# Performance work log

Measured on AMD Instinct MI355X. Metric: run time of the kernel, lower is better.

Reference implementation:

```python
import jax, jax.numpy as jnp
import numpy as np

TEMPERATURE = 0.5
EPS = 1e-8  # torch.nn.CosineSimilarity default eps


def setup_inputs() -> dict:
    key = jax.random.key(0)
    k1, k2 = jax.random.split(key)
    B, D = 4096, 256
    z1 = jax.random.normal(k1, (B, D), dtype=jnp.float32)
    # z2 = perturbed view of z1 so positive cosine sims are positive
    # (original torch code takes log of the RAW cosine sim, which is NaN
    #  for negative positives; realistic SimCLR positives are correlated views)
    z2 = z1 + 0.1 * jax.random.normal(k2, (B, D), dtype=jnp.float32)
    return {"z1": z1, "z2": z2}


def reference(z1, z2):
    B = z1.shape[0]
    z = jnp.concatenate([z1, z2], axis=0)                      # [2B, D]
    norm = jnp.maximum(jnp.linalg.norm(z, axis=-1, keepdims=True), EPS)
    zn = z / norm
    sim = zn @ zn.T                                            # [2B, 2B] cosine sims
    # positives: sim[i, i+B] and sim[i+B, i] (RAW cosine, per original code)
    pos = jnp.concatenate([jnp.diagonal(sim, offset=B),
                           jnp.diagonal(sim, offset=-B)])      # [2B]
    # mask self-similarity diagonal to -inf before exp-sum
    diag = jnp.eye(2 * B, dtype=bool)
    sim_masked = jnp.where(diag, -jnp.inf, sim)
    denom = jnp.sum(jnp.exp(sim_masked / TEMPERATURE), axis=-1)  # [2B]
    loss = -jnp.mean(jnp.log(pos / denom))
    return loss
```

## Files before the change

### kernel.cpp

```cpp
#include <hip/hip_runtime.h>
#include <hip/hip_bf16.h>


#define NROWS 8192
#define BHALF 4096
#define DDIM  256

typedef __attribute__((ext_vector_type(4))) int   i32x4;
typedef __attribute__((ext_vector_type(8))) int   i32x8;
typedef __attribute__((ext_vector_type(4))) float f32x4;

#define SCALE1 0x7F7F7F7F
#define TWO_LOG2E 2.8853900817779268f

__device__ __forceinline__ void load_lds16(const unsigned char* g, unsigned char* l) {
    __builtin_amdgcn_global_load_lds(
        (const __attribute__((address_space(1))) void*)g,
        (__attribute__((address_space(3))) void*)l, 16, 0, 0);
}

__global__ __launch_bounds__(256) void prep_kernel(const float* __restrict__ z1,
                                                   const float* __restrict__ z2,
                                                   unsigned char* __restrict__ zn8,
                                                   float* __restrict__ posPart,
                                                   float* __restrict__ denom,
                                                   float* __restrict__ out) {
    __shared__ float sp[4];
    int wave = threadIdx.x >> 6;
    int lane = threadIdx.x & 63;
    int i    = blockIdx.x * 4 + wave;
    float4 a = reinterpret_cast<const float4*>(z1 + (size_t)i * DDIM)[lane];
    float4 b = reinterpret_cast<const float4*>(z2 + (size_t)i * DDIM)[lane];
    float ss1 = a.x * a.x + a.y * a.y + a.z * a.z + a.w * a.w;
    float ss2 = b.x * b.x + b.y * b.y + b.z * b.z + b.w * b.w;
    float dd  = a.x * b.x + a.y * b.y + a.z * b.z + a.w * b.w;
    #pragma unroll
    for (int off = 32; off; off >>= 1) {
        ss1 += __shfl_xor(ss1, off);
        ss2 += __shfl_xor(ss2, off);
        dd  += __shfl_xor(dd, off);
    }
    float n1 = fmaxf(sqrtf(ss1), 1e-8f);
    float n2 = fmaxf(sqrtf(ss2), 1e-8f);
    float i1 = 1.0f / n1, i2 = 1.0f / n2;
    int pa = __builtin_amdgcn_cvt_pk_fp8_f32(a.x * i1, a.y * i1, 0, 0);
    pa     = __builtin_amdgcn_cvt_pk_fp8_f32(a.z * i1, a.w * i1, pa, 1);
    int pb = __builtin_amdgcn_cvt_pk_fp8_f32(b.x * i2, b.y * i2, 0, 0);
    pb     = __builtin_amdgcn_cvt_pk_fp8_f32(b.z * i2, b.w * i2, pb, 1);
    reinterpret_cast<int*>(zn8 + (size_t)i * DDIM)[lane] = pa;
    reinterpret_cast<int*>(zn8 + (size_t)(i + BHALF) * DDIM)[lane] = pb;
    if (lane == 0) sp[wave] = __logf(dd * i1 * i2);
    if (threadIdx.x < 8) denom[blockIdx.x * 8 + threadIdx.x] = 0.0f;
    if (blockIdx.x == 0 && threadIdx.x == 64) out[0] = 0.0f;
    __syncthreads();
    if (threadIdx.x == 0)
        posPart[blockIdx.x] = sp[0] + sp[1] + sp[2] + sp[3];
}

__global__ __launch_bounds__(256, 3) void denom_kernel(const unsigned char* __restrict__ zn8,
                                                       float* __restrict__ denom) {
    __shared__ __align__(16) unsigned char sMem[48 * 1024];
    unsigned char* sA  = sMem;
    unsigned char* sB0 = sMem + 32768;
    unsigned char* sB1 = sMem;

    int x = blockIdx.x, y = blockIdx.y;
    int bi, bj;
    if (x > y) { bi = y;      bj = x - 1;  }
    else       { bi = 63 - y; bj = 63 - x; }
    int iBase = bi * 128;
    int jBase = bj * 128;
    bool isDiag = (bi == bj);

    int t    = threadIdx.x;
    int lane = t & 63;
    int wave = t >> 6;
    int col  = lane & 15;
    int quad = lane >> 4;
    int wm = wave >> 1, wn = wave & 1;

    int rowL  = t >> 4;
    int chunk = (t & 15) ^ rowL;

    {
        const unsigned char* gA = zn8 + (size_t)(iBase + rowL) * DDIM + chunk * 16;
        #pragma unroll
        for (int q = 0; q < 8; q++)
            load_lds16(gA + q * 4096, sA + t * 16 + q * 4096);
        const unsigned char* gB = zn8 + (size_t)(jBase + rowL) * DDIM + chunk * 16;
        #pragma unroll
        for (int q = 0; q < 4; q++)
            load_lds16(gB + q * 4096, sB0 + t * 16 + q * 4096);
    }
    __syncthreads();

    i32x8 af[4][2];
    {
        const unsigned char* aRow = sA + (size_t)(wm * 64 + col) * DDIM;
        #pragma unroll
        for (int mt = 0; mt < 4; mt++)
            #pragma unroll
            for (int ks = 0; ks < 2; ks++) {
                int g0 = ks * 8 + quad * 2;
                i32x4 lo = *(const i32x4*)(aRow + mt * 16 * DDIM + ((g0    ) ^ col) * 16);
                i32x4 hi = *(const i32x4*)(aRow + mt * 16 * DDIM + ((g0 + 1) ^ col) * 16);
                af[mt][ks] = __builtin_shufflevector(lo, hi, 0, 1, 2, 3, 4, 5, 6, 7);
            }
    }
    __syncthreads();

    {
        const unsigned char* gB = zn8 + (size_t)(jBase + 64 + rowL) * DDIM + chunk * 16;
        #pragma unroll
        for (int q = 0; q < 4; q++)
            load_lds16(gB + q * 4096, sB1 + t * 16 + q * 4096);
    }

    float rs[4][4];
    #pragma unroll
    for (int mt = 0; mt < 4; mt++)
        #pragma unroll
        for (int r = 0; r < 4; r++) rs[mt][r] = 0.f;

    #pragma unroll
    for (int h = 0; h < 2; h++) {
        if (h) __syncthreads();
        const unsigned char* bRow =
            (h ? sB1 : sB0) + (size_t)(wn * 32 + col) * DDIM;

        i32x8 bfr[2][2];
        #pragma unroll
        for (int nt = 0; nt < 2; nt++)
            #pragma unroll
            for (int ks = 0; ks < 2; ks++) {
                int g0 = ks * 8 + quad * 2;
                i32x4 lo = *(const i32x4*)(bRow + nt * 16 * DDIM + ((g0    ) ^ col) * 16);
                i32x4 hi = *(const i32x4*)(bRow + nt * 16 * DDIM + ((g0 + 1) ^ col) * 16);
                bfr[nt][ks] = __builtin_shufflevector(lo, hi, 0, 1, 2, 3, 4, 5, 6, 7);
            }

        float cs[2] = {0.f, 0.f};
        #pragma unroll
        for (int mt = 0; mt < 4; mt++) {
            int gi = iBase + wm * 64 + mt * 16;
            #pragma unroll
            for (int nt = 0; nt < 2; nt++) {
                f32x4 acc = {0.f, 0.f, 0.f, 0.f};
                acc = __builtin_amdgcn_mfma_scale_f32_16x16x128_f8f6f4(
                          af[mt][0], bfr[nt][0], acc, 0, 0, 0, SCALE1, 0, SCALE1);
                acc = __builtin_amdgcn_mfma_scale_f32_16x16x128_f8f6f4(
                          af[mt][1], bfr[nt][1], acc, 0, 0, 0, SCALE1, 0, SCALE1);
                bool dtile = (gi == jBase + h * 64 + wn * 32 + nt * 16);
                float csl = 0.f;
                #pragma unroll
                for (int r = 0; r < 4; r++) {
                    float e = exp2f(acc[r] * TWO_LOG2E);
                    if (dtile && (quad * 4 + r) == col) e = 0.f;
                    rs[mt][r] += e;
                    csl += e;
                }
                cs[nt] += csl;
            }
        }

        if (!isDiag) {
            #pragma unroll
            for (int nt = 0; nt < 2; nt++) {
                float v = cs[nt];
                v += __shfl_xor(v, 16);
                v += __shfl_xor(v, 32);
                if (quad == 0)
                    atomicAdd(&denom[jBase + h * 64 + wn * 32 + nt * 16 + col], v);
            }
        }
    }

    #pragma unroll
    for (int mt = 0; mt < 4; mt++)
        #pragma unroll
        for (int r = 0; r < 4; r++) {
            float v = rs[mt][r];
            v += __shfl_xor(v, 1);
            v += __shfl_xor(v, 2);
            v += __shfl_xor(v, 4);
            v += __shfl_xor(v, 8);
            rs[mt][r] = v;
        }
    __syncthreads();
    float* red = (float*)(sMem + 16384);
    if (col == 0) {
        #pragma unroll
        for (int mt = 0; mt < 4; mt++)
            #pragma unroll
            for (int r = 0; r < 4; r++)
                red[wn * 128 + wm * 64 + mt * 16 + quad * 4 + r] = rs[mt][r];
    }
    __syncthreads();
    if (t < 128)
        atomicAdd(&denom[iBase + t], red[t] + red[128 + t]);
}

__global__ __launch_bounds__(256) void loss_kernel(const float* __restrict__ posPart,
                                                   const float* __restrict__ denom,
                                                   float* __restrict__ out) {
    __shared__ float sdata[4];
    int t = threadIdx.x;
    float s = __logf(denom[blockIdx.x * 256 + t]);
    if (t < 32) s -= 2.0f * posPart[blockIdx.x * 32 + t];
    #pragma unroll
    for (int off = 32; off; off >>= 1) s += __shfl_xor(s, off);
    if ((t & 63) == 0) sdata[t >> 6] = s;
    __syncthreads();
    if (t == 0)
        atomicAdd(out, (sdata[0] + sdata[1] + sdata[2] + sdata[3]) * (1.0f / NROWS));
}

extern "C" void kernel_launch(void* const* d_in, const int* in_sizes, int n_in,
                              void* d_out, int out_size, void* d_ws, size_t ws_size,
                              hipStream_t stream) {
    const float* z1 = (const float*)d_in[0];
    const float* z2 = (const float*)d_in[1];

    unsigned char* zn8 = (unsigned char*)d_ws;
    float* denom   = (float*)((char*)d_ws + (size_t)NROWS * DDIM);
    float* posPart = denom + NROWS;

    prep_kernel<<<BHALF / 4, 256, 0, stream>>>(z1, z2, zn8, posPart, denom, (float*)d_out);
    denom_kernel<<<dim3(65, 32), 256, 0, stream>>>(zn8, denom);
    loss_kernel<<<NROWS / 256, 256, 0, stream>>>(posPart, denom, (float*)d_out);
}
```

Measured before the change: 86.71 us.

## Replace global atomic denominator accumulation with per-tile partial sums array

```diff
diff --git a/kernel.cpp b/kernel.cpp
--- a/kernel.cpp
+++ b/kernel.cpp
@@ -23,7 +23,6 @@
                                                    const float* __restrict__ z2,
                                                    unsigned char* __restrict__ zn8,
                                                    float* __restrict__ posPart,
-                                                   float* __restrict__ denom,
                                                    float* __restrict__ out) {
     __shared__ float sp[4];
     int wave = threadIdx.x >> 6;
@@ -50,7 +49,6 @@
     reinterpret_cast<int*>(zn8 + (size_t)i * DDIM)[lane] = pa;
     reinterpret_cast<int*>(zn8 + (size_t)(i + BHALF) * DDIM)[lane] = pb;
     if (lane == 0) sp[wave] = __logf(dd * i1 * i2);
-    if (threadIdx.x < 8) denom[blockIdx.x * 8 + threadIdx.x] = 0.0f;
     if (blockIdx.x == 0 && threadIdx.x == 64) out[0] = 0.0f;
     __syncthreads();
     if (threadIdx.x == 0)
@@ -58,11 +56,13 @@
 }
 
 __global__ __launch_bounds__(256, 3) void denom_kernel(const unsigned char* __restrict__ zn8,
-                                                       float* __restrict__ denom) {
+                                                       float* __restrict__ P) {
     __shared__ __align__(16) unsigned char sMem[48 * 1024];
     unsigned char* sA  = sMem;
     unsigned char* sB0 = sMem + 32768;
     unsigned char* sB1 = sMem;
+    float* red    = (float*)(sMem + 16384);
+    float* colRed = red + 256;
 
     int x = blockIdx.x, y = blockIdx.y;
     int bi, bj;
@@ -170,7 +170,7 @@
                 v += __shfl_xor(v, 16);
                 v += __shfl_xor(v, 32);
                 if (quad == 0)
-                    atomicAdd(&denom[jBase + h * 64 + wn * 32 + nt * 16 + col], v);
+                    colRed[wm * 128 + h * 64 + wn * 32 + nt * 16 + col] = v;
             }
         }
     }
@@ -187,7 +187,6 @@
             rs[mt][r] = v;
         }
     __syncthreads();
-    float* red = (float*)(sMem + 16384);
     if (col == 0) {
         #pragma unroll
         for (int mt = 0; mt < 4; mt++)
@@ -196,16 +195,33 @@
                 red[wn * 128 + wm * 64 + mt * 16 + quad * 4 + r] = rs[mt][r];
     }
     __syncthreads();
-    if (t < 128)
-        atomicAdd(&denom[iBase + t], red[t] + red[128 + t]);
+    if (t < 128) {
+        float* Prow = P + (((size_t)bi * 64 + bj) << 7);
+        Prow[t] = red[t] + red[128 + t];
+        if (!isDiag) {
+            float* Pcol = P + (((size_t)bj * 64 + bi) << 7);
+            Pcol[t] = colRed[t] + colRed[128 + t];
+        }
+    }
 }
 
 __global__ __launch_bounds__(256) void loss_kernel(const float* __restrict__ posPart,
-                                                   const float* __restrict__ denom,
+                                                   const float* __restrict__ P,
                                                    float* __restrict__ out) {
     __shared__ float sdata[4];
     int t = threadIdx.x;
-    float s = __logf(denom[blockIdx.x * 256 + t]);
+    int i = blockIdx.x * 256 + t;
+    int bi = i >> 7, r = i & 127;
+    const float* p = P + ((size_t)bi << 13) + r;
+    float d0 = 0.f, d1 = 0.f, d2 = 0.f, d3 = 0.f;
+    #pragma unroll
+    for (int k = 0; k < 64; k += 4) {
+        d0 += p[(k + 0) << 7];
+        d1 += p[(k + 1) << 7];
+        d2 += p[(k + 2) << 7];
+        d3 += p[(k + 3) << 7];
+    }
+    float s = __logf((d0 + d1) + (d2 + d3));
     if (t < 32) s -= 2.0f * posPart[blockIdx.x * 32 + t];
     #pragma unroll
     for (int off = 32; off; off >>= 1) s += __shfl_xor(s, off);
@@ -222,10 +238,10 @@
     const float* z2 = (const float*)d_in[1];
 
     unsigned char* zn8 = (unsigned char*)d_ws;
-    float* denom   = (float*)((char*)d_ws + (size_t)NROWS * DDIM);
-    float* posPart = denom + NROWS;
-
-    prep_kernel<<<BHALF / 4, 256, 0, stream>>>(z1, z2, zn8, posPart, denom, (float*)d_out);
-    denom_kernel<<<dim3(65, 32), 256, 0, stream>>>(zn8, denom);
-    loss_kernel<<<NROWS / 256, 256, 0, stream>>>(posPart, denom, (float*)d_out);
-}
+    float* P       = (float*)((char*)d_ws + (size_t)NROWS * DDIM);
+    float* posPart = P + 64 * 64 * 128;
+
+    prep_kernel<<<BHALF / 4, 256, 0, stream>>>(z1, z2, zn8, posPart, (float*)d_out);
+    denom_kernel<<<dim3(65, 32), 256, 0, stream>>>(zn8, P);
+    loss_kernel<<<NROWS / 256, 256, 0, stream>>>(posPart, P, (float*)d_out);
+}
```

Result: no change. 86.59 us (-0.1%).
